# Performance work log

Measured on AMD Instinct MI355X. Metric: run time of the kernel, lower is better.

The kernel has to match this reference:

```python
import jax, jax.numpy as jnp
import numpy as np

EMBED_DIM = 1024
NUM_TOKENS = 32
TOKEN_DIM = 32  # ceil(1024/32)
CODEBOOK_SIZE = 256
BATCH = 32768
BETA = 0.25


def setup_inputs() -> dict:
    key = jax.random.key(0)
    ks = jax.random.split(key, 6)
    lim_e = 1.0 / np.sqrt(EMBED_DIM)
    lim_d = 1.0 / np.sqrt(NUM_TOKENS * TOKEN_DIM)
    lim_c = 1.0 / CODEBOOK_SIZE
    return {
        "skills": jax.random.normal(ks[0], (BATCH, EMBED_DIM), jnp.float32),
        "enc_w": jax.random.uniform(ks[1], (NUM_TOKENS * TOKEN_DIM, EMBED_DIM), jnp.float32, -lim_e, lim_e),
        "enc_b": jax.random.uniform(ks[2], (NUM_TOKENS * TOKEN_DIM,), jnp.float32, -lim_e, lim_e),
        "codebook": jax.random.uniform(ks[3], (CODEBOOK_SIZE, TOKEN_DIM), jnp.float32, -lim_c, lim_c),
        "dec_w": jax.random.uniform(ks[4], (EMBED_DIM, NUM_TOKENS * TOKEN_DIM), jnp.float32, -lim_d, lim_d),
        "dec_b": jax.random.uniform(ks[5], (EMBED_DIM,), jnp.float32, -lim_d, lim_d),
    }


def reference(skills, enc_w, enc_b, codebook, dec_w, dec_b):
    B = skills.shape[0]
    # encoder linear -> [B, num_tokens, token_dim]
    projected = (skills @ enc_w.T + enc_b).reshape(B, NUM_TOKENS, TOKEN_DIM)
    flat = projected.reshape(-1, TOKEN_DIM)  # [B*T, d]
    # squared-euclidean distances to codebook entries: [B*T, K]
    dists = (
        jnp.sum(flat * flat, axis=1, keepdims=True)
        - 2.0 * flat @ codebook.T
        + jnp.sum(codebook * codebook, axis=1)[None, :]
    )
    codes = jnp.argmin(dists, axis=1)  # [B*T]
    quantized = codebook[codes].reshape(B, NUM_TOKENS, TOKEN_DIM)
    # straight-through estimator
    st = projected + jax.lax.stop_gradient(quantized - projected)
    commitment = jnp.mean((projected - jax.lax.stop_gradient(quantized)) ** 2)
    codebook_loss = jnp.mean((quantized - jax.lax.stop_gradient(projected)) ** 2)
    vq_loss = codebook_loss + BETA * commitment
    reconstructed = st.reshape(B, NUM_TOKENS * TOKEN_DIM) @ dec_w.T + dec_b
    recon_loss = jnp.mean((reconstructed - skills) ** 2)
    loss = vq_loss + recon_loss
    return reconstructed, codes.reshape(B, NUM_TOKENS), loss
```

## Files before the change

kernel.cpp:

```cpp
#include <hip/hip_runtime.h>
#include <hip/hip_bf16.h>
#include <float.h>

#define OUT_CODES_OFF (33554432UL)
#define OUT_LOSS_OFF  (34603008UL)
#define TAU 1e-5f
#define INV_N (1.0f/33554432.0f)

typedef __attribute__((ext_vector_type(8))) short s16x8;
typedef __attribute__((ext_vector_type(4))) float f32x4;

__device__ __forceinline__ unsigned short bf16r(float x) {
    unsigned int u = __float_as_uint(x);
    unsigned int r = (u + 0x7FFFu + ((u >> 16) & 1u)) >> 16;
    return (unsigned short)r;
}
__device__ __forceinline__ float bf16f(unsigned short h) {
    return __uint_as_float(((unsigned int)h) << 16);
}
__device__ __forceinline__ void split8r(float4 v0, float4 v1, s16x8& h, s16x8& l) {
    float xs[8] = {v0.x, v0.y, v0.z, v0.w, v1.x, v1.y, v1.z, v1.w};
    #pragma unroll
    for (int e = 0; e < 8; ++e) {
        unsigned int u = __float_as_uint(xs[e]);
        unsigned short hh = (unsigned short)(u >> 16);
        h[e] = (short)hh;
        l[e] = (short)bf16r(xs[e] - bf16f(hh));
    }
}

__global__ void k_prep_r(const float* __restrict__ in,
                         unsigned short* __restrict__ o,
                         int n8)
{
    const int i = blockIdx.x * 256 + threadIdx.x;
    if (i >= n8) return;
    const float4* p = (const float4*)(in + (size_t)i * 8);
    float4 v0 = p[0], v1 = p[1];
    float xs[8] = {v0.x, v0.y, v0.z, v0.w, v1.x, v1.y, v1.z, v1.w};
    s16x8 h;
    #pragma unroll
    for (int e = 0; e < 8; ++e) h[e] = (short)bf16r(xs[e]);
    *(s16x8*)(o + (size_t)i * 8) = h;
}

__launch_bounds__(512, 1)
__global__ void k_enc(const float* __restrict__ skills,
                      const float* __restrict__ enc_w,
                      const float* __restrict__ enc_b,
                      const float* __restrict__ cb_g,
                      float* __restrict__ out)
{
    __shared__ __align__(16) char smem[125952];
    typedef unsigned short (*pu40)[40];
    pu40 Ah = (pu40)(smem);
    pu40 Al = (pu40)(smem + 10240);
    pu40 Bh = (pu40)(smem + 20480);
    pu40 Bl = (pu40)(smem + 30720);
    pu40 Sh = (pu40)(smem);
    pu40 Sl = (pu40)(smem + 40960);
    pu40 Ch = (pu40)(smem + 81920);
    pu40 Cl = (pu40)(smem + 102400);
    float* cnb = (float*)(smem + 122880);
    float* Fv  = (float*)(smem + 123904);

    const int tid = threadIdx.x;
    const int r0 = blockIdx.x * 128;
    const int wid = tid >> 6, lane = tid & 63;
    const int wm = wid >> 1, wn = wid & 1;
    const int mbase = wm * 32, nbase = wn * 64;
    const int lhi = lane >> 4, llo = lane & 15;
    const int srow = tid >> 2, sq = tid & 3;

    if (tid < 256) {
        const float4* cr = (const float4*)&cb_g[tid * 32];
        float s = 0.f;
        #pragma unroll
        for (int i = 0; i < 8; ++i) {
            float4 v = cr[i];
            float c[4] = {v.x, v.y, v.z, v.w};
            #pragma unroll
            for (int e = 0; e < 4; ++e) {
                unsigned int u = __float_as_uint(c[e]);
                unsigned short hh = (unsigned short)(u >> 16);
                Ch[tid][i*4+e] = hh;
                Cl[tid][i*4+e] = bf16r(c[e] - bf16f(hh));
                s = fmaf(c[e], c[e], s);
            }
        }
        cnb[tid] = s;
    }
    __syncthreads();

    float vq_local = 0.f;
    f32x4 acc[2][4];
    float4 ra0, ra1, rb0, rb1;

    {
        const float* ap = &skills[(size_t)(r0 + srow) * 1024 + sq * 8];
        ra0 = *(const float4*)ap; ra1 = *(const float4*)(ap + 4);
        const float* bp = &enc_w[(size_t)srow * 1024 + sq * 8];
        rb0 = *(const float4*)bp; rb1 = *(const float4*)(bp + 4);
    }

    for (int it = 0; it < 256; ++it) {
        const int nt = it >> 5, kt = it & 31;
        const int n0 = nt * 128;
        if (kt == 0) {
            #pragma unroll
            for (int mf = 0; mf < 2; ++mf)
                #pragma unroll
                for (int nf = 0; nf < 4; ++nf) acc[mf][nf] = (f32x4)0.f;
        }
        __syncthreads();
        {
            s16x8 h, l;
            split8r(ra0, ra1, h, l);
            *(s16x8*)&Ah[srow][sq * 8] = h;
            *(s16x8*)&Al[srow][sq * 8] = l;
            split8r(rb0, rb1, h, l);
            *(s16x8*)&Bh[srow][sq * 8] = h;
            *(s16x8*)&Bl[srow][sq * 8] = l;
        }
        __syncthreads();
        if (it < 255) {
            const int it2 = it + 1, nt2 = it2 >> 5, kt2 = it2 & 31;
            const float* ap = &skills[(size_t)(r0 + srow) * 1024 + kt2 * 32 + sq * 8];
            ra0 = *(const float4*)ap; ra1 = *(const float4*)(ap + 4);
            const float* bp = &enc_w[(size_t)(nt2 * 128 + srow) * 1024 + kt2 * 32 + sq * 8];
            rb0 = *(const float4*)bp; rb1 = *(const float4*)(bp + 4);
        }
        {
            s16x8 ah[2], al[2], bh[4], bl[4];
            #pragma unroll
            for (int mf = 0; mf < 2; ++mf) {
                const int row = mbase + mf * 16 + llo;
                ah[mf] = *(s16x8*)&Ah[row][lhi * 8];
                al[mf] = *(s16x8*)&Al[row][lhi * 8];
            }
            #pragma unroll
            for (int nf = 0; nf < 4; ++nf) {
                const int row = nbase + nf * 16 + llo;
                bh[nf] = *(s16x8*)&Bh[row][lhi * 8];
                bl[nf] = *(s16x8*)&Bl[row][lhi * 8];
            }
            #pragma unroll
            for (int mf = 0; mf < 2; ++mf)
                #pragma unroll
                for (int nf = 0; nf < 4; ++nf) {
                    acc[mf][nf] = __builtin_amdgcn_mfma_f32_16x16x32_bf16(ah[mf], bh[nf], acc[mf][nf], 0, 0, 0);
                    acc[mf][nf] = __builtin_amdgcn_mfma_f32_16x16x32_bf16(ah[mf], bl[nf], acc[mf][nf], 0, 0, 0);
                    acc[mf][nf] = __builtin_amdgcn_mfma_f32_16x16x32_bf16(al[mf], bh[nf], acc[mf][nf], 0, 0, 0);
                }
        }

        if (kt == 31) {
            __syncthreads();
            float fp[2][4][2];
            #pragma unroll
            for (int mf = 0; mf < 2; ++mf)
                #pragma unroll
                for (int r = 0; r < 4; ++r) { fp[mf][r][0] = 0.f; fp[mf][r][1] = 0.f; }

            #pragma unroll
            for (int mf = 0; mf < 2; ++mf)
                #pragma unroll
                for (int nf = 0; nf < 4; ++nf) {
                    const int n_local = nbase + nf * 16 + llo;
                    const float bias = enc_b[n0 + n_local];
                    const int tl = wn * 2 + (nf >> 1);
                    const int d = ((nf & 1) << 4) + llo;
                    #pragma unroll
                    for (int r = 0; r < 4; ++r) {
                        const int m_local = mbase + mf * 16 + lhi * 4 + r;
                        float val = acc[mf][nf][r] + bias;
                        unsigned int u = __float_as_uint(val);
                        unsigned short hh = (unsigned short)(u >> 16);
                        Sh[m_local * 4 + tl][d] = hh;
                        Sl[m_local * 4 + tl][d] = bf16r(val - bf16f(hh));
                        fp[mf][r][nf >> 1] = fmaf(val, val, fp[mf][r][nf >> 1]);
                    }
                }
            #pragma unroll
            for (int mf = 0; mf < 2; ++mf)
                #pragma unroll
                for (int r = 0; r < 4; ++r)
                    #pragma unroll
                    for (int tt = 0; tt < 2; ++tt) {
                        float f = fp[mf][r][tt];
                        f += __shfl_xor(f, 1); f += __shfl_xor(f, 2);
                        f += __shfl_xor(f, 4); f += __shfl_xor(f, 8);
                        if (llo == 0)
                            Fv[(mbase + mf * 16 + lhi * 4 + r) * 4 + wn * 2 + tt] = f;
                    }
            __syncthreads();

            #pragma unroll
            for (int gi = 0; gi < 4; ++gi) {
                const int g = wid * 4 + gi;
                const int tokrow = g * 16 + llo;
                s16x8 fh = *(s16x8*)&Sh[tokrow][lhi * 8];
                s16x8 fl = *(s16x8*)&Sl[tokrow][lhi * 8];
                float s1[4], s2[4]; int bj[4];
                #pragma unroll
                for (int r = 0; r < 4; ++r) { s1[r] = FLT_MAX; s2[r] = FLT_MAX; bj[r] = 0; }
                for (int jb = 0; jb < 16; ++jb) {
                    const int j = jb * 16 + llo;
                    s16x8 ch = *(s16x8*)&Ch[j][lhi * 8];
                    s16x8 cl = *(s16x8*)&Cl[j][lhi * 8];
                    f32x4 sc = (f32x4)0.f;
                    sc = __builtin_amdgcn_mfma_f32_16x16x32_bf16(fh, ch, sc, 0, 0, 0);
                    sc = __builtin_amdgcn_mfma_f32_16x16x32_bf16(fh, cl, sc, 0, 0, 0);
                    sc = __builtin_amdgcn_mfma_f32_16x16x32_bf16(fl, ch, sc, 0, 0, 0);
                    const float cnv = cnb[j];
                    #pragma unroll
                    for (int r = 0; r < 4; ++r) {
                        float s = fmaf(-2.f, sc[r], cnv);
                        if (s < s1[r])      { s2[r] = s1[r]; s1[r] = s; bj[r] = j; }
                        else if (s < s2[r]) { s2[r] = s; }
                    }
                }
                #pragma unroll
                for (int r = 0; r < 4; ++r) {
                    float a1 = s1[r], a2 = s2[r]; int aj = bj[r];
                    #pragma unroll
                    for (int off = 1; off <= 8; off <<= 1) {
                        float o1 = __shfl_xor(a1, off);
                        float o2 = __shfl_xor(a2, off);
                        int   oj = __shfl_xor(aj, off);
                        if (o1 < a1) { a2 = fminf(a1, o2); a1 = o1; aj = oj; }
                        else         { a2 = fminf(o1, a2); }
                    }
                    if (llo == 0) {
                        const int tok_local = g * 16 + lhi * 4 + r;
                        const float F = Fv[tok_local];
                        float cv = (a2 - a1 < TAU) ? (float)(aj + 512) : (float)aj;
                        const size_t tok = (size_t)(r0 + (tok_local >> 2)) * 32 + nt * 4 + (tok_local & 3);
                        out[OUT_CODES_OFF + tok] = cv;
                        vq_local += F + a1;
                    }
                }
            }
        }
    }
    {
        float v = vq_local;
        #pragma unroll
        for (int off = 32; off >= 1; off >>= 1) v += __shfl_xor(v, off);
        if (lane == 0) atomicAdd(&out[OUT_LOSS_OFF], v * (1.25f * INV_N));
    }
}

__launch_bounds__(256)
__global__ void k_fix(const float* __restrict__ skills,
                      const float* __restrict__ enc_w,
                      const float* __restrict__ enc_b,
                      const float* __restrict__ cb_g,
                      float* __restrict__ codes)
{
    __shared__ unsigned int cnt;
    __shared__ unsigned short list[256];

    const int tid = threadIdx.x;
    const int base = blockIdx.x * 256;

    if (tid == 0) cnt = 0;
    __syncthreads();
    {
        const int c = (int)codes[base + tid];
        if (c >= 512) {
            unsigned int ix = atomicAdd(&cnt, 1u);
            list[ix] = (unsigned short)tid;
        }
    }
    __syncthreads();
    const unsigned int n = cnt;
    if (n == 0) return;

    const int wv = tid >> 6, lane = tid & 63;
    const int d = lane & 31;

    for (unsigned int i = wv; i < n; i += 4) {
        const int tok = base + (int)list[i];
        const int row = tok >> 5;
        const int t   = tok & 31;

        const float4* s4 = (const float4*)&skills[(size_t)row * 1024];
        const float4* w4 = (const float4*)&enc_w[(size_t)(t * 32 + d) * 1024];
        float v1 = 0.f, v2 = 0.f, v3 = 0.f;
        for (int q = 0; q < 96; ++q) {
            float4 a = s4[q], b = w4[q];
            v1 = fmaf(a.x, b.x, v1); v1 = fmaf(a.y, b.y, v1);
            v1 = fmaf(a.z, b.z, v1); v1 = fmaf(a.w, b.w, v1);
        }
        for (int q = 96; q < 192; ++q) {
            float4 a = s4[q], b = w4[q];
            v2 = fmaf(a.x, b.x, v2); v2 = fmaf(a.y, b.y, v2);
            v2 = fmaf(a.z, b.z, v2); v2 = fmaf(a.w, b.w, v2);
        }
        for (int q = 192; q < 256; ++q) {
            float4 a = s4[q], b = w4[q];
            v3 = fmaf(a.x, b.x, v3); v3 = fmaf(a.y, b.y, v3);
            v3 = fmaf(a.z, b.z, v3); v3 = fmaf(a.w, b.w, v3);
        }
        const float pd = ((v1 + v2) + v3) + enc_b[t * 32 + d];

        float pv[32];
        #pragma unroll
        for (int dd = 0; dd < 32; ++dd) pv[dd] = __shfl(pd, dd);

        float F;
        {
            float s[32];
            #pragma unroll
            for (int dd = 0; dd < 32; ++dd) s[dd] = pv[dd] * pv[dd];
            float r[8];
            #pragma unroll
            for (int j = 0; j < 8; ++j) r[j] = ((s[j] + s[8+j]) + s[16+j]) + s[24+j];
            F = ((r[0] + r[1]) + (r[2] + r[3])) + ((r[4] + r[5]) + (r[6] + r[7]));
        }

        float bs = FLT_MAX; int bj = 0;
        for (int m = 0; m < 4; ++m) {
            const int j = m * 64 + lane;
            const float* cj = &cb_g[j * 32];
            float g = 0.f;
            #pragma unroll
            for (int dd = 0; dd < 32; ++dd) g = fmaf(pv[dd], cj[dd], g);
            float cs[32];
            #pragma unroll
            for (int dd = 0; dd < 32; ++dd) cs[dd] = cj[dd] * cj[dd];
            float r[8];
            #pragma unroll
            for (int jj = 0; jj < 8; ++jj) r[jj] = ((cs[jj] + cs[8+jj]) + cs[16+jj]) + cs[24+jj];
            float cn = ((r[0] + r[1]) + (r[2] + r[3])) + ((r[4] + r[5]) + (r[6] + r[7]));
            float dist = (F - 2.0f * g) + cn;
            if (dist < bs) { bs = dist; bj = j; }
        }
        #pragma unroll
        for (int off = 32; off >= 1; off >>= 1) {
            float os = __shfl_xor(bs, off);
            int   oj = __shfl_xor(bj, off);
            if (os < bs || (os == bs && oj < bj)) { bs = os; bj = oj; }
        }
        if (lane == 0) codes[tok] = (float)bj;
    }
}

template <bool PRED>
__launch_bounds__(512)
__global__ void k_dec(const float* __restrict__ skills,
                      const float* __restrict__ cb_g,
                      const unsigned short* __restrict__ cbb,
                      const float* __restrict__ dec_w,
                      const unsigned short* __restrict__ dwb,
                      const float* __restrict__ dec_b,
                      const float* __restrict__ codes,
                      float* __restrict__ recon,
                      float* __restrict__ loss_out)
{
    __shared__ unsigned short Qt[128][40], Wt[128][40];

    const int tid = threadIdx.x;
    const int r0 = (blockIdx.x >> 3) * 128;
    const int n0 = (blockIdx.x & 7) * 128;
    const int wid = tid >> 6, lane = tid & 63;
    const int wm = wid >> 1, wn = wid & 1;
    const int mbase = wm * 32, nbase = wn * 64;
    const int lhi = lane >> 4, llo = lane & 15;
    const int srow = tid >> 2, sq = tid & 3;

    f32x4 acc[2][4];
    #pragma unroll
    for (int mf = 0; mf < 2; ++mf)
        #pragma unroll
        for (int nf = 0; nf < 4; ++nf) acc[mf][nf] = (f32x4)0.f;

    s16x8 q16, w16;
    float4 q0, q1, w0, w1;
    int cnext;
    {
        const int c0 = ((int)codes[(size_t)(r0 + srow) * 32 + 0]) & 255;
        if (PRED) {
            q16 = *(const s16x8*)(cbb + c0 * 32 + sq * 8);
            w16 = *(const s16x8*)(dwb + (size_t)(n0 + srow) * 1024 + sq * 8);
        } else {
            const float* cp = &cb_g[c0 * 32 + sq * 8];
            q0 = *(const float4*)cp; q1 = *(const float4*)(cp + 4);
            const float* wp = &dec_w[(size_t)(n0 + srow) * 1024 + sq * 8];
            w0 = *(const float4*)wp; w1 = *(const float4*)(wp + 4);
        }
        cnext = ((int)codes[(size_t)(r0 + srow) * 32 + 1]) & 255;
    }

    for (int t = 0; t < 32; ++t) {
        __syncthreads();
        if (PRED) {
            *(s16x8*)&Qt[srow][sq * 8] = q16;
            *(s16x8*)&Wt[srow][sq * 8] = w16;
        } else {
            float xs[8] = {q0.x, q0.y, q0.z, q0.w, q1.x, q1.y, q1.z, q1.w};
            s16x8 h;
            #pragma unroll
            for (int e = 0; e < 8; ++e) h[e] = (short)bf16r(xs[e]);
            *(s16x8*)&Qt[srow][sq * 8] = h;
            float ys[8] = {w0.x, w0.y, w0.z, w0.w, w1.x, w1.y, w1.z, w1.w};
            #pragma unroll
            for (int e = 0; e < 8; ++e) h[e] = (short)bf16r(ys[e]);
            *(s16x8*)&Wt[srow][sq * 8] = h;
        }
        __syncthreads();
        if (t < 31) {
            if (PRED) {
                q16 = *(const s16x8*)(cbb + cnext * 32 + sq * 8);
                w16 = *(const s16x8*)(dwb + (size_t)(n0 + srow) * 1024 + (t + 1) * 32 + sq * 8);
            } else {
                const float* cp = &cb_g[cnext * 32 + sq * 8];
                q0 = *(const float4*)cp; q1 = *(const float4*)(cp + 4);
                const float* wp = &dec_w[(size_t)(n0 + srow) * 1024 + (t + 1) * 32 + sq * 8];
                w0 = *(const float4*)wp; w1 = *(const float4*)(wp + 4);
            }
            if (t < 30) cnext = ((int)codes[(size_t)(r0 + srow) * 32 + t + 2]) & 255;
        }
        s16x8 aq[2], bw[4];
        #pragma unroll
        for (int mf = 0; mf < 2; ++mf)
            aq[mf] = *(s16x8*)&Qt[mbase + mf * 16 + llo][lhi * 8];
        #pragma unroll
        for (int nf = 0; nf < 4; ++nf)
            bw[nf] = *(s16x8*)&Wt[nbase + nf * 16 + llo][lhi * 8];
        #pragma unroll
        for (int mf = 0; mf < 2; ++mf)
            #pragma unroll
            for (int nf = 0; nf < 4; ++nf)
                acc[mf][nf] = __builtin_amdgcn_mfma_f32_16x16x32_bf16(aq[mf], bw[nf], acc[mf][nf], 0, 0, 0);
    }

    float lsum = 0.f;
    #pragma unroll
    for (int mf = 0; mf < 2; ++mf)
        #pragma unroll
        for (int nf = 0; nf < 4; ++nf) {
            const int col = n0 + nbase + nf * 16 + llo;
            const float bias = dec_b[col];
            #pragma unroll
            for (int r = 0; r < 4; ++r) {
                const int row = r0 + mbase + mf * 16 + lhi * 4 + r;
                float rv = acc[mf][nf][r] + bias;
                float dv = rv - skills[(size_t)row * 1024 + col];
                lsum = fmaf(dv, dv, lsum);
                recon[(size_t)row * 1024 + col] = rv;
            }
        }
    #pragma unroll
    for (int off = 32; off >= 1; off >>= 1) lsum += __shfl_xor(lsum, off);
    if (lane == 0) atomicAdd(loss_out, lsum * INV_N);
}

extern "C" void kernel_launch(void* const* d_in, const int* in_sizes, int n_in,
                              void* d_out, int out_size, void* d_ws, size_t ws_size,
                              hipStream_t stream)
{
    const float* skills = (const float*)d_in[0];
    const float* enc_w  = (const float*)d_in[1];
    const float* enc_b  = (const float*)d_in[2];
    const float* cbg    = (const float*)d_in[3];
    const float* dec_w  = (const float*)d_in[4];
    const float* dec_b  = (const float*)d_in[5];
    float* out = (float*)d_out;

    hipMemsetAsync(out + OUT_LOSS_OFF, 0, 4, stream);
    k_enc<<<dim3(256), dim3(512), 0, stream>>>(skills, enc_w, enc_b, cbg, out);
    k_fix<<<dim3(4096), dim3(256), 0, stream>>>(skills, enc_w, enc_b, cbg, out + OUT_CODES_OFF);

    const bool pred = (ws_size >= (2097152UL + 16384UL + 64UL));
    unsigned short* dwb = (unsigned short*)d_ws;
    unsigned short* cbb = dwb + 1048576UL;
    if (pred) {
        k_prep_r<<<dim3(512), dim3(256), 0, stream>>>(dec_w, dwb, 131072);
        k_prep_r<<<dim3(4), dim3(256), 0, stream>>>(cbg, cbb, 1024);
        k_dec<true><<<dim3(2048), dim3(512), 0, stream>>>(skills, cbg, cbb, dec_w, dwb, dec_b,
                                                          out + OUT_CODES_OFF, out, out + OUT_LOSS_OFF);
    } else {
        k_dec<false><<<dim3(2048), dim3(512), 0, stream>>>(skills, cbg, cbb, dec_w, dwb, dec_b,
                                                           out + OUT_CODES_OFF, out, out + OUT_LOSS_OFF);
    }
}
```

Baseline: 918.2 us.

## Split encoder across column halves and shrink shared memory for higher occupancy

The encoder kernel now launches twice as many blocks, with each block covering half of the 1024 output columns for its 128 rows. Shared memory drops from about 123KB to 80KB by packing the codebook norms into the padding of the codebook rows and by running the distance epilogue in two column passes. The token norm is now recomputed from the bf16 hi/lo split instead of from the fp32 values. Launch bounds are raised to allow several blocks per CU, which may cause register spills, and each skills tile is now loaded by two blocks instead of one.

```diff
diff --git a/kernel.cpp b/kernel.cpp
--- a/kernel.cpp
+++ b/kernel.cpp
@@ -44,31 +44,21 @@
     *(s16x8*)(o + (size_t)i * 8) = h;
 }
 
-__launch_bounds__(512, 1)
+__launch_bounds__(512, 4)
 __global__ void k_enc(const float* __restrict__ skills,
                       const float* __restrict__ enc_w,
                       const float* __restrict__ enc_b,
                       const float* __restrict__ cb_g,
                       float* __restrict__ out)
 {
-    __shared__ __align__(16) char smem[125952];
-    typedef unsigned short (*pu40)[40];
-    pu40 Ah = (pu40)(smem);
-    pu40 Al = (pu40)(smem + 10240);
-    pu40 Bh = (pu40)(smem + 20480);
-    pu40 Bl = (pu40)(smem + 30720);
-    pu40 Sh = (pu40)(smem);
-    pu40 Sl = (pu40)(smem + 40960);
-    pu40 Ch = (pu40)(smem + 81920);
-    pu40 Cl = (pu40)(smem + 102400);
-    float* cnb = (float*)(smem + 122880);
-    float* Fv  = (float*)(smem + 123904);
+    __shared__ __align__(16) unsigned short us[40960];
 
     const int tid = threadIdx.x;
-    const int r0 = blockIdx.x * 128;
+    const int rb = blockIdx.x >> 1, chf = blockIdx.x & 1;
+    const int r0 = rb * 128;
     const int wid = tid >> 6, lane = tid & 63;
     const int wm = wid >> 1, wn = wid & 1;
-    const int mbase = wm * 32, nbase = wn * 64;
+    const int mbase = wm * 32;
     const int lhi = lane >> 4, llo = lane & 15;
     const int srow = tid >> 2, sq = tid & 3;
 
@@ -81,14 +71,15 @@
             float c[4] = {v.x, v.y, v.z, v.w};
             #pragma unroll
             for (int e = 0; e < 4; ++e) {
+                const int d = i * 4 + e;
                 unsigned int u = __float_as_uint(c[e]);
                 unsigned short hh = (unsigned short)(u >> 16);
-                Ch[tid][i*4+e] = hh;
-                Cl[tid][i*4+e] = bf16r(c[e] - bf16f(hh));
+                us[20480 + tid * 40 + d] = hh;
+                us[30720 + tid * 40 + d] = bf16r(c[e] - bf16f(hh));
                 s = fmaf(c[e], c[e], s);
             }
         }
-        cnb[tid] = s;
+        *(float*)&us[20480 + tid * 40 + 32] = s;
     }
     __syncthreads();
 
@@ -99,13 +90,12 @@
     {
         const float* ap = &skills[(size_t)(r0 + srow) * 1024 + sq * 8];
         ra0 = *(const float4*)ap; ra1 = *(const float4*)(ap + 4);
-        const float* bp = &enc_w[(size_t)srow * 1024 + sq * 8];
+        const float* bp = &enc_w[(size_t)(chf * 512 + srow) * 1024 + sq * 8];
         rb0 = *(const float4*)bp; rb1 = *(const float4*)(bp + 4);
     }
 
-    for (int it = 0; it < 256; ++it) {
+    for (int it = 0; it < 128; ++it) {
         const int nt = it >> 5, kt = it & 31;
-        const int n0 = nt * 128;
         if (kt == 0) {
             #pragma unroll
             for (int mf = 0; mf < 2; ++mf)
@@ -116,128 +106,120 @@
         {
             s16x8 h, l;
             split8r(ra0, ra1, h, l);
-            *(s16x8*)&Ah[srow][sq * 8] = h;
-            *(s16x8*)&Al[srow][sq * 8] = l;
+            *(s16x8*)&us[srow * 40 + sq * 8] = h;
+            *(s16x8*)&us[5120 + srow * 40 + sq * 8] = l;
             split8r(rb0, rb1, h, l);
-            *(s16x8*)&Bh[srow][sq * 8] = h;
-            *(s16x8*)&Bl[srow][sq * 8] = l;
+            *(s16x8*)&us[10240 + srow * 40 + sq * 8] = h;
+            *(s16x8*)&us[15360 + srow * 40 + sq * 8] = l;
         }
         __syncthreads();
-        if (it < 255) {
+        if (it < 127) {
             const int it2 = it + 1, nt2 = it2 >> 5, kt2 = it2 & 31;
             const float* ap = &skills[(size_t)(r0 + srow) * 1024 + kt2 * 32 + sq * 8];
             ra0 = *(const float4*)ap; ra1 = *(const float4*)(ap + 4);
-            const float* bp = &enc_w[(size_t)(nt2 * 128 + srow) * 1024 + kt2 * 32 + sq * 8];
+            const float* bp = &enc_w[(size_t)(chf * 512 + nt2 * 128 + srow) * 1024 + kt2 * 32 + sq * 8];
             rb0 = *(const float4*)bp; rb1 = *(const float4*)(bp + 4);
         }
         {
-            s16x8 ah[2], al[2], bh[4], bl[4];
+            s16x8 ah[2], al[2];
             #pragma unroll
             for (int mf = 0; mf < 2; ++mf) {
                 const int row = mbase + mf * 16 + llo;
-                ah[mf] = *(s16x8*)&Ah[row][lhi * 8];
-                al[mf] = *(s16x8*)&Al[row][lhi * 8];
+                ah[mf] = *(s16x8*)&us[row * 40 + lhi * 8];
+                al[mf] = *(s16x8*)&us[5120 + row * 40 + lhi * 8];
             }
             #pragma unroll
             for (int nf = 0; nf < 4; ++nf) {
-                const int row = nbase + nf * 16 + llo;
-                bh[nf] = *(s16x8*)&Bh[row][lhi * 8];
-                bl[nf] = *(s16x8*)&Bl[row][lhi * 8];
-            }
-            #pragma unroll
-            for (int mf = 0; mf < 2; ++mf)
+                const int rowb = wn * 64 + nf * 16 + llo;
+                s16x8 bh = *(s16x8*)&us[10240 + rowb * 40 + lhi * 8];
+                s16x8 bl = *(s16x8*)&us[15360 + rowb * 40 + lhi * 8];
                 #pragma unroll
-                for (int nf = 0; nf < 4; ++nf) {
-                    acc[mf][nf] = __builtin_amdgcn_mfma_f32_16x16x32_bf16(ah[mf], bh[nf], acc[mf][nf], 0, 0, 0);
-                    acc[mf][nf] = __builtin_amdgcn_mfma_f32_16x16x32_bf16(ah[mf], bl[nf], acc[mf][nf], 0, 0, 0);
-                    acc[mf][nf] = __builtin_amdgcn_mfma_f32_16x16x32_bf16(al[mf], bh[nf], acc[mf][nf], 0, 0, 0);
+                for (int mf = 0; mf < 2; ++mf) {
+                    acc[mf][nf] = __builtin_amdgcn_mfma_f32_16x16x32_bf16(ah[mf], bh, acc[mf][nf], 0, 0, 0);
+                    acc[mf][nf] = __builtin_amdgcn_mfma_f32_16x16x32_bf16(ah[mf], bl, acc[mf][nf], 0, 0, 0);
+                    acc[mf][nf] = __builtin_amdgcn_mfma_f32_16x16x32_bf16(al[mf], bh, acc[mf][nf], 0, 0, 0);
                 }
+            }
         }
 
         if (kt == 31) {
-            __syncthreads();
-            float fp[2][4][2];
-            #pragma unroll
-            for (int mf = 0; mf < 2; ++mf)
+            for (int c = 0; c < 2; ++c) {
+                __syncthreads();
+                if (wn == c) {
+                    #pragma unroll
+                    for (int nf = 0; nf < 4; ++nf) {
+                        const int colh = nf * 16 + llo;
+                        const int tlc = colh >> 5, d = colh & 31;
+                        const float bias = enc_b[chf * 512 + nt * 128 + c * 64 + colh];
+                        #pragma unroll
+                        for (int mf = 0; mf < 2; ++mf)
+                            #pragma unroll
+                            for (int r = 0; r < 4; ++r) {
+                                const int m_local = mbase + mf * 16 + lhi * 4 + r;
+                                float val = acc[mf][nf][r] + bias;
+                                unsigned int u = __float_as_uint(val);
+                                unsigned short hh = (unsigned short)(u >> 16);
+                                const int tok = m_local * 2 + tlc;
+                                us[tok * 40 + d] = hh;
+                                us[10240 + tok * 40 + d] = bf16r(val - bf16f(hh));
+                            }
+                    }
+                }
+                __syncthreads();
                 #pragma unroll
-                for (int r = 0; r < 4; ++r) { fp[mf][r][0] = 0.f; fp[mf][r][1] = 0.f; }
-
-            #pragma unroll
-            for (int mf = 0; mf < 2; ++mf)
-                #pragma unroll
-                for (int nf = 0; nf < 4; ++nf) {
-                    const int n_local = nbase + nf * 16 + llo;
-                    const float bias = enc_b[n0 + n_local];
-                    const int tl = wn * 2 + (nf >> 1);
-                    const int d = ((nf & 1) << 4) + llo;
+                for (int gi = 0; gi < 2; ++gi) {
+                    const int g = wid * 2 + gi;
+                    const int tokrow = g * 16 + llo;
+                    s16x8 fh = *(s16x8*)&us[tokrow * 40 + lhi * 8];
+                    s16x8 fl = *(s16x8*)&us[10240 + tokrow * 40 + lhi * 8];
+                    float Fp = 0.f;
+                    #pragma unroll
+                    for (int e = 0; e < 8; ++e) {
+                        float fv = bf16f((unsigned short)fh[e]) + bf16f((unsigned short)fl[e]);
+                        Fp = fmaf(fv, fv, Fp);
+                    }
+                    Fp += __shfl_xor(Fp, 16);
+                    Fp += __shfl_xor(Fp, 32);
+
+                    float s1[4], s2[4]; int bj[4];
+                    #pragma unroll
+                    for (int r = 0; r < 4; ++r) { s1[r] = FLT_MAX; s2[r] = FLT_MAX; bj[r] = 0; }
+                    for (int jb = 0; jb < 16; ++jb) {
+                        const int j = jb * 16 + llo;
+                        s16x8 ch = *(s16x8*)&us[20480 + j * 40 + lhi * 8];
+                        s16x8 cl = *(s16x8*)&us[30720 + j * 40 + lhi * 8];
+                        const float cnv = *(const float*)&us[20480 + j * 40 + 32];
+                        f32x4 sc = (f32x4)0.f;
+                        sc = __builtin_amdgcn_mfma_f32_16x16x32_bf16(fh, ch, sc, 0, 0, 0);
+                        sc = __builtin_amdgcn_mfma_f32_16x16x32_bf16(fh, cl, sc, 0, 0, 0);
+                        sc = __builtin_amdgcn_mfma_f32_16x16x32_bf16(fl, ch, sc, 0, 0, 0);
+                        #pragma unroll
+                        for (int r = 0; r < 4; ++r) {
+                            float s = fmaf(-2.f, sc[r], cnv);
+                            if (s < s1[r])      { s2[r] = s1[r]; s1[r] = s; bj[r] = j; }
+                            else if (s < s2[r]) { s2[r] = s; }
+                        }
+                    }
                     #pragma unroll
                     for (int r = 0; r < 4; ++r) {
-                        const int m_local = mbase + mf * 16 + lhi * 4 + r;
-                        float val = acc[mf][nf][r] + bias;
-                        unsigned int u = __float_as_uint(val);
-                        unsigned short hh = (unsigned short)(u >> 16);
-                        Sh[m_local * 4 + tl][d] = hh;
-                        Sl[m_local * 4 + tl][d] = bf16r(val - bf16f(hh));
-                        fp[mf][r][nf >> 1] = fmaf(val, val, fp[mf][r][nf >> 1]);
-                    }
-                }
-            #pragma unroll
-            for (int mf = 0; mf < 2; ++mf)
-                #pragma unroll
-                for (int r = 0; r < 4; ++r)
-                    #pragma unroll
-                    for (int tt = 0; tt < 2; ++tt) {
-                        float f = fp[mf][r][tt];
-                        f += __shfl_xor(f, 1); f += __shfl_xor(f, 2);
-                        f += __shfl_xor(f, 4); f += __shfl_xor(f, 8);
-                        if (llo == 0)
-                            Fv[(mbase + mf * 16 + lhi * 4 + r) * 4 + wn * 2 + tt] = f;
-                    }
-            __syncthreads();
-
-            #pragma unroll
-            for (int gi = 0; gi < 4; ++gi) {
-                const int g = wid * 4 + gi;
-                const int tokrow = g * 16 + llo;
-                s16x8 fh = *(s16x8*)&Sh[tokrow][lhi * 8];
-                s16x8 fl = *(s16x8*)&Sl[tokrow][lhi * 8];
-                float s1[4], s2[4]; int bj[4];
-                #pragma unroll
-                for (int r = 0; r < 4; ++r) { s1[r] = FLT_MAX; s2[r] = FLT_MAX; bj[r] = 0; }
-                for (int jb = 0; jb < 16; ++jb) {
-                    const int j = jb * 16 + llo;
-                    s16x8 ch = *(s16x8*)&Ch[j][lhi * 8];
-                    s16x8 cl = *(s16x8*)&Cl[j][lhi * 8];
-                    f32x4 sc = (f32x4)0.f;
-                    sc = __builtin_amdgcn_mfma_f32_16x16x32_bf16(fh, ch, sc, 0, 0, 0);
-                    sc = __builtin_amdgcn_mfma_f32_16x16x32_bf16(fh, cl, sc, 0, 0, 0);
-                    sc = __builtin_amdgcn_mfma_f32_16x16x32_bf16(fl, ch, sc, 0, 0, 0);
-                    const float cnv = cnb[j];
-                    #pragma unroll
-                    for (int r = 0; r < 4; ++r) {
-                        float s = fmaf(-2.f, sc[r], cnv);
-                        if (s < s1[r])      { s2[r] = s1[r]; s1[r] = s; bj[r] = j; }
-                        else if (s < s2[r]) { s2[r] = s; }
-                    }
-                }
-                #pragma unroll
-                for (int r = 0; r < 4; ++r) {
-                    float a1 = s1[r], a2 = s2[r]; int aj = bj[r];
-                    #pragma unroll
-                    for (int off = 1; off <= 8; off <<= 1) {
-                        float o1 = __shfl_xor(a1, off);
-                        float o2 = __shfl_xor(a2, off);
-                        int   oj = __shfl_xor(aj, off);
-                        if (o1 < a1) { a2 = fminf(a1, o2); a1 = o1; aj = oj; }
-                        else         { a2 = fminf(o1, a2); }
-                    }
-                    if (llo == 0) {
-                        const int tok_local = g * 16 + lhi * 4 + r;
-                        const float F = Fv[tok_local];
-                        float cv = (a2 - a1 < TAU) ? (float)(aj + 512) : (float)aj;
-                        const size_t tok = (size_t)(r0 + (tok_local >> 2)) * 32 + nt * 4 + (tok_local & 3);
-                        out[OUT_CODES_OFF + tok] = cv;
-                        vq_local += F + a1;
+                        float a1 = s1[r], a2 = s2[r]; int aj = bj[r];
+                        #pragma unroll
+                        for (int off = 1; off <= 8; off <<= 1) {
+                            float o1 = __shfl_xor(a1, off);
+                            float o2 = __shfl_xor(a2, off);
+                            int   oj = __shfl_xor(aj, off);
+                            if (o1 < a1) { a2 = fminf(a1, o2); a1 = o1; aj = oj; }
+                            else         { a2 = fminf(o1, a2); }
+                        }
+                        const float Ft = __shfl(Fp, lhi * 4 + r);
+                        if (llo == 0) {
+                            const int tok_local = g * 16 + lhi * 4 + r;
+                            const int row = tok_local >> 1, tlc2 = tok_local & 1;
+                            const int t = chf * 16 + nt * 4 + c * 2 + tlc2;
+                            float cv = (a2 - a1 < TAU) ? (float)(aj + 512) : (float)aj;
+                            out[OUT_CODES_OFF + (size_t)(r0 + row) * 32 + t] = cv;
+                            vq_local += Ft + a1;
+                        }
                     }
                 }
             }
@@ -470,7 +452,7 @@
     float* out = (float*)d_out;
 
     hipMemsetAsync(out + OUT_LOSS_OFF, 0, 4, stream);
-    k_enc<<<dim3(256), dim3(512), 0, stream>>>(skills, enc_w, enc_b, cbg, out);
+    k_enc<<<dim3(512), dim3(512), 0, stream>>>(skills, enc_w, enc_b, cbg, out);
     k_fix<<<dim3(4096), dim3(256), 0, stream>>>(skills, enc_w, enc_b, cbg, out + OUT_CODES_OFF);
 
     const bool pred = (ws_size >= (2097152UL + 16384UL + 64UL));
```

Result: slower. 1.352 ms (+47.2%).
